# Kernel optimization log

Measured on AMD Instinct MI355X. Metric: run time of the kernel, lower is better.

Reference implementation:

```python
import jax, jax.numpy as jnp
import numpy as np

LEVELS = 2
BS = 8                 # block_size == plane_h == plane_w
NORMALS = (0, 1, 2)    # axis-aligned plane normals within each block
TAU = 0.05
INV_SQRT2 = 0.7071067811865476

# ---------- 1D orthonormal Haar along an axis ----------

def _dwt1(x, axis):
    x = jnp.moveaxis(x, axis, -1)
    a, b = x[..., 0::2], x[..., 1::2]
    lo = (a + b) * INV_SQRT2
    hi = (a - b) * INV_SQRT2
    return jnp.moveaxis(lo, -1, axis), jnp.moveaxis(hi, -1, axis)


def _idwt1(lo, hi, axis):
    lo = jnp.moveaxis(lo, axis, -1)
    hi = jnp.moveaxis(hi, axis, -1)
    even = (lo + hi) * INV_SQRT2
    odd = (lo - hi) * INV_SQRT2
    y = jnp.stack([even, odd], axis=-1).reshape(lo.shape[:-1] + (lo.shape[-1] * 2,))
    return jnp.moveaxis(y, -1, axis)

# ---------- one level of separable 3D Haar (8 subbands) ----------

def _dwt3_level(x):
    ld, hd = _dwt1(x, -3)
    out = {}
    for dn, db in (('l', ld), ('h', hd)):
        lh, hh = _dwt1(db, -2)
        for hn, hb in (('l', lh), ('h', hh)):
            lw, hw = _dwt1(hb, -1)
            out[dn + hn + 'l'] = lw
            out[dn + hn + 'h'] = hw
    return out


def _idwt3_level(bands):
    rec_h = {dn + hn: _idwt1(bands[dn + hn + 'l'], bands[dn + hn + 'h'], -1)
             for dn in 'lh' for hn in 'lh'}
    rec_d = {dn: _idwt1(rec_h[dn + 'l'], rec_h[dn + 'h'], -2) for dn in 'lh'}
    return _idwt1(rec_d['l'], rec_d['h'], -3)

# ---------- full multi-level 2D Haar on the last two dims (planes) ----------

def _haar2_fwd(p):
    s = p.shape[-1]
    out = p
    while s > 1:
        sub = out[..., :s, :s]
        a, b = sub[..., 0::2, :], sub[..., 1::2, :]
        sub = jnp.concatenate([(a + b) * INV_SQRT2, (a - b) * INV_SQRT2], axis=-2)
        a, b = sub[..., :, 0::2], sub[..., :, 1::2]
        sub = jnp.concatenate([(a + b) * INV_SQRT2, (a - b) * INV_SQRT2], axis=-1)
        out = out.at[..., :s, :s].set(sub)
        s //= 2
    return out


def _haar2_inv(c):
    s_full = c.shape[-1]
    out = c
    s = 2
    while s <= s_full:
        sub = out[..., :s, :s]
        lo, hi = sub[..., :, :s // 2], sub[..., :, s // 2:]
        even = (lo + hi) * INV_SQRT2
        odd = (lo - hi) * INV_SQRT2
        sub = jnp.stack([even, odd], axis=-1).reshape(sub.shape[:-1] + (s,))
        lo, hi = sub[..., :s // 2, :], sub[..., s // 2:, :]
        even = (lo + hi) * INV_SQRT2
        odd = (lo - hi) * INV_SQRT2
        sub = jnp.stack([even, odd], axis=-2).reshape(sub.shape[:-2] + (s, s))
        out = out.at[..., :s, :s].set(sub)
        s *= 2
    return out

# ---------- block extraction / assembly ----------

def _extract_blocks(band, bs):
    B, C, D, H, W = band.shape
    pd, ph, pw = (-D) % bs, (-H) % bs, (-W) % bs
    band = jnp.pad(band, ((0, 0), (0, 0), (0, pd), (0, ph), (0, pw)), mode='edge')
    nd, nh, nw = (D + pd) // bs, (H + ph) // bs, (W + pw) // bs
    blk = band.reshape(B, C, nd, bs, nh, bs, nw, bs).transpose(0, 1, 2, 4, 6, 3, 5, 7)
    return blk.reshape(-1, bs, bs, bs), (B, C, D, H, W), (nd, nh, nw)


def _assemble_blocks(blocks, orig, nblk, bs):
    B, C, D, H, W = orig
    nd, nh, nw = nblk
    x = blocks.reshape(B, C, nd, nh, nw, bs, bs, bs).transpose(0, 1, 2, 5, 3, 6, 4, 7)
    x = x.reshape(B, C, nd * bs, nh * bs, nw * bs)
    return x[:, :, :D, :H, :W]

# ---------- planewise bandlet analysis / synthesis ----------

def _analyze(blocks):
    # for each normal axis n: slice cube into planes perpendicular to n, 2D Haar each plane
    return jnp.stack([_haar2_fwd(jnp.moveaxis(blocks, 1 + n, 1)) for n in NORMALS], axis=1)


def _synthesize(packed):
    recs = [jnp.moveaxis(_haar2_inv(packed[:, i]), 1, 1 + n) for i, n in enumerate(NORMALS)]
    acc = recs[0]
    for r in recs[1:]:
        acc = acc + r
    return acc / len(NORMALS)


def _soft_threshold(c, tau):
    dc = c[..., 0, 0]  # keep per-plane DC coefficient
    t = jnp.sign(c) * jnp.maximum(jnp.abs(c) - tau, 0.0)
    return t.at[..., 0, 0].set(dc)

# ---------- full encode -> threshold -> reconstruct ----------

def _forward(x):
    B, C, D, H, W = x.shape
    mult = 2 ** LEVELS
    pd, ph, pw = (-D) % mult, (-H) % mult, (-W) % mult
    xp = jnp.pad(x, ((0, 0), (0, 0), (0, pd), (0, ph), (0, pw)), mode='reflect')
    approx = xp
    levels = []
    for _ in range(LEVELS):
        bands = _dwt3_level(approx)
        approx = bands.pop('lll')
        levels.append(bands)
    rec_levels = []
    for bands in levels:
        rec = {}
        for name, band in bands.items():
            blocks, orig, nblk = _extract_blocks(band, BS)
            packed = _soft_threshold(_analyze(blocks), TAU)
            rec[name] = _assemble_blocks(_synthesize(packed), orig, nblk, BS)
        rec_levels.append(rec)
    y = approx
    for bands in reversed(rec_levels):
        bands = dict(bands)
        bands['lll'] = y
        y = _idwt3_level(bands)
    return y[:, :, :D, :H, :W]


def setup_inputs() -> dict:
    key = jax.random.key(0)
    x = jax.random.normal(key, (2, 1, 160, 160, 160), dtype=jnp.float32)
    return {"x": x}


def reference(x):
    return _forward(x)
```

## Files before the change

kernel.cpp:

```cpp
#include <hip/hip_runtime.h>

#define IS2 0.7071067811865476f
#define C3F 0.35355339059327373f
#define TAU_F 0.05f

__device__ __forceinline__ void haar2_fwd(float (&m)[64]) {
    float t[64];
    #pragma unroll
    for (int half = 4; half >= 1; half >>= 1) {
        const int sz = half * 2;
        #pragma unroll
        for (int r = 0; r < half; ++r)
            #pragma unroll
            for (int c = 0; c < sz; ++c) {
                float a = m[(2*r)*8 + c], b = m[(2*r+1)*8 + c];
                t[r*8 + c]        = (a + b) * IS2;
                t[(r+half)*8 + c] = (a - b) * IS2;
            }
        #pragma unroll
        for (int r = 0; r < sz; ++r)
            #pragma unroll
            for (int c = 0; c < sz; ++c) m[r*8+c] = t[r*8+c];
        #pragma unroll
        for (int r = 0; r < sz; ++r)
            #pragma unroll
            for (int c = 0; c < half; ++c) {
                float a = m[r*8 + 2*c], b = m[r*8 + 2*c + 1];
                t[r*8 + c]        = (a + b) * IS2;
                t[r*8 + c + half] = (a - b) * IS2;
            }
        #pragma unroll
        for (int r = 0; r < sz; ++r)
            #pragma unroll
            for (int c = 0; c < sz; ++c) m[r*8+c] = t[r*8+c];
    }
}

__device__ __forceinline__ void haar2_inv(float (&m)[64]) {
    float t[64];
    #pragma unroll
    for (int sz = 2; sz <= 8; sz <<= 1) {
        const int half = sz >> 1;
        #pragma unroll
        for (int r = 0; r < sz; ++r)
            #pragma unroll
            for (int c = 0; c < half; ++c) {
                float lo = m[r*8 + c], hi = m[r*8 + c + half];
                t[r*8 + 2*c]     = (lo + hi) * IS2;
                t[r*8 + 2*c + 1] = (lo - hi) * IS2;
            }
        #pragma unroll
        for (int r = 0; r < sz; ++r)
            #pragma unroll
            for (int c = 0; c < sz; ++c) m[r*8+c] = t[r*8+c];
        #pragma unroll
        for (int r = 0; r < half; ++r)
            #pragma unroll
            for (int c = 0; c < sz; ++c) {
                float lo = m[r*8 + c], hi = m[(r+half)*8 + c];
                t[(2*r)*8 + c]   = (lo + hi) * IS2;
                t[(2*r+1)*8 + c] = (lo - hi) * IS2;
            }
        #pragma unroll
        for (int r = 0; r < sz; ++r)
            #pragma unroll
            for (int c = 0; c < sz; ++c) m[r*8+c] = t[r*8+c];
    }
}

__device__ __forceinline__ void bandlet_slice(float (&m)[64]) {
    haar2_fwd(m);
    float dc = m[0];
    #pragma unroll
    for (int e = 0; e < 64; ++e) {
        float v = m[e];
        float av = fabsf(v) - TAU_F;
        m[e] = av > 0.0f ? copysignf(av, v) : 0.0f;
    }
    m[0] = dc;
    haar2_inv(m);
}

__device__ __forceinline__ void bandlet_core(float* __restrict__ L, int s,
                                             bool valid, float (&a)[64]) {
    float g[64], w[64];
    if (valid) {
        #pragma unroll
        for (int r = 0; r < 8; ++r) {
            float4 v0 = *(const float4*)&L[s*64 + r*8];
            float4 v1 = *(const float4*)&L[s*64 + r*8 + 4];
            a[r*8+0]=v0.x; a[r*8+1]=v0.y; a[r*8+2]=v0.z; a[r*8+3]=v0.w;
            a[r*8+4]=v1.x; a[r*8+5]=v1.y; a[r*8+6]=v1.z; a[r*8+7]=v1.w;
        }
        bandlet_slice(a);
        #pragma unroll
        for (int r = 0; r < 8; ++r)
            #pragma unroll
            for (int c = 0; c < 8; ++c)
                g[r*8+c] = L[r*64 + c*8 + s];
        bandlet_slice(g);
        #pragma unroll
        for (int r = 0; r < 8; ++r) {
            float4 v0 = *(const float4*)&L[r*64 + s*8];
            float4 v1 = *(const float4*)&L[r*64 + s*8 + 4];
            w[r*8+0]=v0.x; w[r*8+1]=v0.y; w[r*8+2]=v0.z; w[r*8+3]=v0.w;
            w[r*8+4]=v1.x; w[r*8+5]=v1.y; w[r*8+6]=v1.z; w[r*8+7]=v1.w;
        }
    }
    __syncthreads();
    if (valid) {
        #pragma unroll
        for (int r = 0; r < 8; ++r)
            #pragma unroll
            for (int c = 0; c < 8; ++c)
                L[r*64 + c*8 + s] = g[r*8+c];
        bandlet_slice(w);
    }
    __syncthreads();
    if (valid) {
        #pragma unroll
        for (int r = 0; r < 8; ++r) {
            float4 v0 = *(const float4*)&L[s*64 + r*8];
            float4 v1 = *(const float4*)&L[s*64 + r*8 + 4];
            a[r*8+0]+=v0.x; a[r*8+1]+=v0.y; a[r*8+2]+=v0.z; a[r*8+3]+=v0.w;
            a[r*8+4]+=v1.x; a[r*8+5]+=v1.y; a[r*8+6]+=v1.z; a[r*8+7]+=v1.w;
        }
    }
    __syncthreads();
    if (valid) {
        #pragma unroll
        for (int r = 0; r < 8; ++r) {
            *(float4*)&L[r*64 + s*8]     = make_float4(w[r*8+0], w[r*8+1], w[r*8+2], w[r*8+3]);
            *(float4*)&L[r*64 + s*8 + 4] = make_float4(w[r*8+4], w[r*8+5], w[r*8+6], w[r*8+7]);
        }
    }
    __syncthreads();
    if (valid) {
        #pragma unroll
        for (int r = 0; r < 8; ++r) {
            float4 v0 = *(const float4*)&L[s*64 + r*8];
            float4 v1 = *(const float4*)&L[s*64 + r*8 + 4];
            a[r*8+0]+=v0.x; a[r*8+1]+=v0.y; a[r*8+2]+=v0.z; a[r*8+3]+=v0.w;
            a[r*8+4]+=v1.x; a[r*8+5]+=v1.y; a[r*8+6]+=v1.z; a[r*8+7]+=v1.w;
        }
    }
}

__global__ __launch_bounds__(64, 2) void fwd1_bp(const float* __restrict__ x,
                                                 float* __restrict__ bands) {
    constexpr int LST = 516;
    constexpr size_t B1S = (size_t)2 * 80 * 80 * 80;
    __shared__ __align__(16) float lin[7 * LST];

    const int t  = threadIdx.x;
    const int wg = blockIdx.x;
    const int b  = wg / 1000;
    const int tl = wg - b * 1000;
    const int td = tl / 100;
    const int rr = tl - td * 100;
    const int th = rr / 10;
    const int tw = rr - th * 10;
    const int j = t >> 3, w = t & 7;

    const float* ip = x + ((size_t)(b*160 + 16*td)) * 25600 + (size_t)(16*th) * 160 + 16*tw;
    float* lllp = bands + ((size_t)(b*80 + 8*td)) * 6400 + (size_t)(8*th) * 80 + 8*tw;

    #pragma unroll
    for (int q = 0; q < 8; ++q) {
        const float* p = ip + (size_t)(2*q) * 25600 + (2*j) * 160 + 2*w;
        float2 q00 = *(const float2*)(p);
        float2 q01 = *(const float2*)(p + 160);
        float2 q10 = *(const float2*)(p + 25600);
        float2 q11 = *(const float2*)(p + 25600 + 160);
        float wl00 = q00.x + q00.y, wh00 = q00.x - q00.y;
        float wl01 = q01.x + q01.y, wh01 = q01.x - q01.y;
        float wl10 = q10.x + q10.y, wh10 = q10.x - q10.y;
        float wl11 = q11.x + q11.y, wh11 = q11.x - q11.y;
        float hl0l = wl00 + wl01, hh0l = wl00 - wl01;
        float hl0h = wh00 + wh01, hh0h = wh00 - wh01;
        float hl1l = wl10 + wl11, hh1l = wl10 - wl11;
        float hl1h = wh10 + wh11, hh1h = wh10 - wh11;
        const int pos = q*64 + j*8 + w;
        lin[0*LST + pos] = (hl0h + hl1h) * C3F;
        lin[1*LST + pos] = (hh0l + hh1l) * C3F;
        lin[2*LST + pos] = (hh0h + hh1h) * C3F;
        lin[3*LST + pos] = (hl0l - hl1l) * C3F;
        lin[4*LST + pos] = (hl0h - hl1h) * C3F;
        lin[5*LST + pos] = (hh0l - hh1l) * C3F;
        lin[6*LST + pos] = (hh0h - hh1h) * C3F;
        lllp[q*6400 + j*80 + w] = (hl0l + hl1l) * C3F;
    }
    __syncthreads();

    const int nbp = t >> 3, s = t & 7;
    const bool valid = nbp < 7;
    float a[64];
    bandlet_core(&lin[(valid ? nbp : 0) * LST], s, valid, a);

    if (valid) {
        float* gp = bands + (size_t)(nbp + 1) * B1S
                  + ((size_t)(b*80 + 8*td + s)) * 6400 + (size_t)(8*th) * 80 + 8*tw;
        #pragma unroll
        for (int jj = 0; jj < 8; ++jj) {
            float* qo = gp + jj * 80;
            *(float4*)(qo)     = make_float4(a[jj*8+0]*(1.0f/3.0f), a[jj*8+1]*(1.0f/3.0f),
                                             a[jj*8+2]*(1.0f/3.0f), a[jj*8+3]*(1.0f/3.0f));
            *(float4*)(qo + 4) = make_float4(a[jj*8+4]*(1.0f/3.0f), a[jj*8+5]*(1.0f/3.0f),
                                             a[jj*8+6]*(1.0f/3.0f), a[jj*8+7]*(1.0f/3.0f));
        }
    }
}

__global__ __launch_bounds__(64, 2) void l2_pipeline(float* __restrict__ lll) {
    constexpr int LST = 516;
    __shared__ __align__(16) float lin[8 * LST];

    const int t  = threadIdx.x;
    const int wg = blockIdx.x;
    const int b  = wg / 125;
    const int tl = wg - b * 125;
    const int td = tl / 25;
    const int rr = tl - td * 25;
    const int th = rr / 5;
    const int tw = rr - th * 5;
    const int j = t >> 3, w = t & 7;

    float* base = lll + ((size_t)(b*80 + 16*td)) * 6400 + (size_t)(16*th) * 80 + 16*tw;

    #pragma unroll
    for (int q = 0; q < 8; ++q) {
        const float* p = base + (size_t)(2*q) * 6400 + (2*j) * 80 + 2*w;
        float2 q00 = *(const float2*)(p);
        float2 q01 = *(const float2*)(p + 80);
        float2 q10 = *(const float2*)(p + 6400);
        float2 q11 = *(const float2*)(p + 6400 + 80);
        float wl00 = q00.x + q00.y, wh00 = q00.x - q00.y;
        float wl01 = q01.x + q01.y, wh01 = q01.x - q01.y;
        float wl10 = q10.x + q10.y, wh10 = q10.x - q10.y;
        float wl11 = q11.x + q11.y, wh11 = q11.x - q11.y;
        float hl0l = wl00 + wl01, hh0l = wl00 - wl01;
        float hl0h = wh00 + wh01, hh0h = wh00 - wh01;
        float hl1l = wl10 + wl11, hh1l = wl10 - wl11;
        float hl1h = wh10 + wh11, hh1h = wh10 - wh11;
        const int pos = q*64 + j*8 + w;
        lin[0*LST + pos] = (hl0l + hl1l) * C3F;
        lin[1*LST + pos] = (hl0h + hl1h) * C3F;
        lin[2*LST + pos] = (hh0l + hh1l) * C3F;
        lin[3*LST + pos] = (hh0h + hh1h) * C3F;
        lin[4*LST + pos] = (hl0l - hl1l) * C3F;
        lin[5*LST + pos] = (hl0h - hl1h) * C3F;
        lin[6*LST + pos] = (hh0l - hh1l) * C3F;
        lin[7*LST + pos] = (hh0h - hh1h) * C3F;
    }
    __syncthreads();

    const int nbp = t >> 3, s = t & 7;
    const bool valid = nbp < 7;
    float a[64];
    bandlet_core(&lin[(valid ? nbp + 1 : 0) * LST], s, valid, a);

    __syncthreads();
    if (valid) {
        float* L = &lin[(nbp + 1) * LST];
        #pragma unroll
        for (int jj = 0; jj < 8; ++jj) {
            *(float4*)&L[s*64 + jj*8]     = make_float4(a[jj*8+0]*(1.0f/3.0f), a[jj*8+1]*(1.0f/3.0f),
                                                        a[jj*8+2]*(1.0f/3.0f), a[jj*8+3]*(1.0f/3.0f));
            *(float4*)&L[s*64 + jj*8 + 4] = make_float4(a[jj*8+4]*(1.0f/3.0f), a[jj*8+5]*(1.0f/3.0f),
                                                        a[jj*8+6]*(1.0f/3.0f), a[jj*8+7]*(1.0f/3.0f));
        }
    }
    __syncthreads();

    #pragma unroll
    for (int q = 0; q < 8; ++q) {
        const int pos = q*64 + j*8 + w;
        float b0 = lin[0*LST + pos], b1 = lin[1*LST + pos];
        float b2 = lin[2*LST + pos], b3 = lin[3*LST + pos];
        float b4 = lin[4*LST + pos], b5 = lin[5*LST + pos];
        float b6 = lin[6*LST + pos], b7 = lin[7*LST + pos];
        float c0 = b0 + b4, c1 = b1 + b5, c2 = b2 + b6, c3 = b3 + b7;
        float c4 = b0 - b4, c5 = b1 - b5, c6 = b2 - b6, c7 = b3 - b7;
        float e00 = c0 + c2, e01 = c1 + c3;
        float e02 = c0 - c2, e03 = c1 - c3;
        float e10 = c4 + c6, e11 = c5 + c7;
        float e12 = c4 - c6, e13 = c5 - c7;
        float* pp = base + (size_t)(2*q) * 6400 + (2*j) * 80 + 2*w;
        *(float2*)(pp)             = make_float2((e00+e01)*C3F, (e00-e01)*C3F);
        *(float2*)(pp + 80)        = make_float2((e02+e03)*C3F, (e02-e03)*C3F);
        *(float2*)(pp + 6400)      = make_float2((e10+e11)*C3F, (e10-e11)*C3F);
        *(float2*)(pp + 6400 + 80) = make_float2((e12+e13)*C3F, (e12-e13)*C3F);
    }
}

__global__ __launch_bounds__(256) void dwt3_inv80(const float* __restrict__ bands,
                                                  float* __restrict__ out) {
    const int tid = blockIdx.x * blockDim.x + threadIdx.x;
    constexpr int S = 80;
    const int w = tid % S;
    const int h = (tid / S) % S;
    const int d = (tid / (S*S)) % S;
    const int b = tid / (S*S*S);
    constexpr size_t bs_ = (size_t)2 * S * S * S;
    const size_t o = (size_t)tid;

    float b0 = bands[0*bs_+o], b1 = bands[1*bs_+o], b2 = bands[2*bs_+o], b3 = bands[3*bs_+o];
    float b4 = bands[4*bs_+o], b5 = bands[5*bs_+o], b6 = bands[6*bs_+o], b7 = bands[7*bs_+o];
    float c0 = b0 + b4, c1 = b1 + b5, c2 = b2 + b6, c3 = b3 + b7;
    float c4 = b0 - b4, c5 = b1 - b5, c6 = b2 - b6, c7 = b3 - b7;
    float e00 = c0 + c2, e01 = c1 + c3;
    float e02 = c0 - c2, e03 = c1 - c3;
    float e10 = c4 + c6, e11 = c5 + c7;
    float e12 = c4 - c6, e13 = c5 - c7;
    constexpr int IS = 2 * S;
    float* p = out + (((size_t)b * IS + 2*d) * IS + 2*h) * IS + 2*w;
    *(float2*)(p)                      = make_float2((e00+e01)*C3F, (e00-e01)*C3F);
    *(float2*)(p + IS)                 = make_float2((e02+e03)*C3F, (e02-e03)*C3F);
    *(float2*)(p + (size_t)IS*IS)      = make_float2((e10+e11)*C3F, (e10-e11)*C3F);
    *(float2*)(p + (size_t)IS*IS + IS) = make_float2((e12+e13)*C3F, (e12-e13)*C3F);
}

extern "C" void kernel_launch(void* const* d_in, const int* in_sizes, int n_in,
                              void* d_out, int out_size, void* d_ws, size_t ws_size,
                              hipStream_t stream) {
    const float* x = (const float*)d_in[0];
    float* out = (float*)d_out;
    float* bands = (float*)d_ws;

    fwd1_bp<<<2000, 64, 0, stream>>>(x, bands);
    l2_pipeline<<<250, 64, 0, stream>>>(bands);
    dwt3_inv80<<<4000, 256, 0, stream>>>(bands, out);
}
```

Before: 119.3 us.

## Split three bandlet orientations across three wavefronts and widen inverse DWT per thread

Each workgroup now runs 192 threads, so each of the three plane orientations of the bandlet transform gets its own wavefront instead of one thread processing all three serially. The second orientation's result is routed through an extra shared buffer and summed by wave 0. The Haar 2D transforms use smaller temporaries to cut register pressure. The final inverse DWT processes two outputs per thread with float2 loads and float4 stores. Shared memory per block roughly doubles, and 8 of every 64 lanes in each wave stay idle, which may limit occupancy.

New measurement: 120.3 us. No clear change (+0.8%).

```diff
diff --git a/kernel.cpp b/kernel.cpp
--- a/kernel.cpp
+++ b/kernel.cpp
@@ -3,68 +3,68 @@
 #define IS2 0.7071067811865476f
 #define C3F 0.35355339059327373f
 #define TAU_F 0.05f
+#define THIRD 0.3333333333333333f
 
 __device__ __forceinline__ void haar2_fwd(float (&m)[64]) {
-    float t[64];
     #pragma unroll
     for (int half = 4; half >= 1; half >>= 1) {
         const int sz = half * 2;
+        float th[32];
         #pragma unroll
         for (int r = 0; r < half; ++r)
             #pragma unroll
             for (int c = 0; c < sz; ++c) {
                 float a = m[(2*r)*8 + c], b = m[(2*r+1)*8 + c];
-                t[r*8 + c]        = (a + b) * IS2;
-                t[(r+half)*8 + c] = (a - b) * IS2;
-            }
-        #pragma unroll
-        for (int r = 0; r < sz; ++r)
-            #pragma unroll
-            for (int c = 0; c < sz; ++c) m[r*8+c] = t[r*8+c];
-        #pragma unroll
-        for (int r = 0; r < sz; ++r)
+                m[r*8 + c] = (a + b) * IS2;
+                th[r*8 + c] = (a - b) * IS2;
+            }
+        #pragma unroll
+        for (int r = 0; r < half; ++r)
+            #pragma unroll
+            for (int c = 0; c < sz; ++c) m[(r+half)*8 + c] = th[r*8 + c];
+        #pragma unroll
+        for (int r = 0; r < sz; ++r) {
+            float tw[4];
             #pragma unroll
             for (int c = 0; c < half; ++c) {
                 float a = m[r*8 + 2*c], b = m[r*8 + 2*c + 1];
-                t[r*8 + c]        = (a + b) * IS2;
-                t[r*8 + c + half] = (a - b) * IS2;
-            }
-        #pragma unroll
-        for (int r = 0; r < sz; ++r)
-            #pragma unroll
-            for (int c = 0; c < sz; ++c) m[r*8+c] = t[r*8+c];
+                m[r*8 + c] = (a + b) * IS2;
+                tw[c]      = (a - b) * IS2;
+            }
+            #pragma unroll
+            for (int c = 0; c < half; ++c) m[r*8 + c + half] = tw[c];
+        }
     }
 }
 
 __device__ __forceinline__ void haar2_inv(float (&m)[64]) {
-    float t[64];
     #pragma unroll
     for (int sz = 2; sz <= 8; sz <<= 1) {
         const int half = sz >> 1;
         #pragma unroll
-        for (int r = 0; r < sz; ++r)
+        for (int r = 0; r < sz; ++r) {
+            float te[8];
             #pragma unroll
             for (int c = 0; c < half; ++c) {
                 float lo = m[r*8 + c], hi = m[r*8 + c + half];
-                t[r*8 + 2*c]     = (lo + hi) * IS2;
-                t[r*8 + 2*c + 1] = (lo - hi) * IS2;
-            }
-        #pragma unroll
-        for (int r = 0; r < sz; ++r)
-            #pragma unroll
-            for (int c = 0; c < sz; ++c) m[r*8+c] = t[r*8+c];
-        #pragma unroll
-        for (int r = 0; r < half; ++r)
-            #pragma unroll
-            for (int c = 0; c < sz; ++c) {
+                te[2*c]   = (lo + hi) * IS2;
+                te[2*c+1] = (lo - hi) * IS2;
+            }
+            #pragma unroll
+            for (int k = 0; k < sz; ++k) m[r*8 + k] = te[k];
+        }
+        #pragma unroll
+        for (int c = 0; c < sz; ++c) {
+            float tc[8];
+            #pragma unroll
+            for (int r = 0; r < half; ++r) {
                 float lo = m[r*8 + c], hi = m[(r+half)*8 + c];
-                t[(2*r)*8 + c]   = (lo + hi) * IS2;
-                t[(2*r+1)*8 + c] = (lo - hi) * IS2;
-            }
-        #pragma unroll
-        for (int r = 0; r < sz; ++r)
-            #pragma unroll
-            for (int c = 0; c < sz; ++c) m[r*8+c] = t[r*8+c];
+                tc[2*r]   = (lo + hi) * IS2;
+                tc[2*r+1] = (lo - hi) * IS2;
+            }
+            #pragma unroll
+            for (int r = 0; r < sz; ++r) m[r*8 + c] = tc[r];
+        }
     }
 }
 
@@ -81,76 +81,74 @@
     haar2_inv(m);
 }
 
-__device__ __forceinline__ void bandlet_core(float* __restrict__ L, int s,
-                                             bool valid, float (&a)[64]) {
-    float g[64], w[64];
-    if (valid) {
+__device__ __forceinline__ void blockproc3(float* __restrict__ Lb,
+                                           float* __restrict__ Rb,
+                                           int wv, int s, bool act,
+                                           float (&m)[64]) {
+    if (act) {
+        if (wv == 0) {
+            #pragma unroll
+            for (int r = 0; r < 8; ++r) {
+                float4 v0 = *(const float4*)&Lb[s*64 + r*8];
+                float4 v1 = *(const float4*)&Lb[s*64 + r*8 + 4];
+                m[r*8+0]=v0.x; m[r*8+1]=v0.y; m[r*8+2]=v0.z; m[r*8+3]=v0.w;
+                m[r*8+4]=v1.x; m[r*8+5]=v1.y; m[r*8+6]=v1.z; m[r*8+7]=v1.w;
+            }
+        } else if (wv == 1) {
+            #pragma unroll
+            for (int r = 0; r < 8; ++r) {
+                float4 v0 = *(const float4*)&Lb[r*64 + s*8];
+                float4 v1 = *(const float4*)&Lb[r*64 + s*8 + 4];
+                m[r*8+0]=v0.x; m[r*8+1]=v0.y; m[r*8+2]=v0.z; m[r*8+3]=v0.w;
+                m[r*8+4]=v1.x; m[r*8+5]=v1.y; m[r*8+6]=v1.z; m[r*8+7]=v1.w;
+            }
+        } else {
+            #pragma unroll
+            for (int r = 0; r < 8; ++r)
+                #pragma unroll
+                for (int c = 0; c < 8; ++c)
+                    m[r*8+c] = Lb[r*64 + c*8 + s];
+        }
+    }
+    __syncthreads();
+    if (act) {
+        bandlet_slice(m);
+        if (wv == 1) {
+            #pragma unroll
+            for (int r = 0; r < 8; ++r) {
+                *(float4*)&Lb[r*64 + s*8]     = make_float4(m[r*8+0], m[r*8+1], m[r*8+2], m[r*8+3]);
+                *(float4*)&Lb[r*64 + s*8 + 4] = make_float4(m[r*8+4], m[r*8+5], m[r*8+6], m[r*8+7]);
+            }
+        } else if (wv == 2) {
+            #pragma unroll
+            for (int r = 0; r < 8; ++r)
+                #pragma unroll
+                for (int c = 0; c < 8; ++c)
+                    Rb[r*64 + c*8 + s] = m[r*8+c];
+        }
+    }
+    __syncthreads();
+    if (act && wv == 0) {
         #pragma unroll
         for (int r = 0; r < 8; ++r) {
-            float4 v0 = *(const float4*)&L[s*64 + r*8];
-            float4 v1 = *(const float4*)&L[s*64 + r*8 + 4];
-            a[r*8+0]=v0.x; a[r*8+1]=v0.y; a[r*8+2]=v0.z; a[r*8+3]=v0.w;
-            a[r*8+4]=v1.x; a[r*8+5]=v1.y; a[r*8+6]=v1.z; a[r*8+7]=v1.w;
-        }
-        bandlet_slice(a);
-        #pragma unroll
-        for (int r = 0; r < 8; ++r)
-            #pragma unroll
-            for (int c = 0; c < 8; ++c)
-                g[r*8+c] = L[r*64 + c*8 + s];
-        bandlet_slice(g);
-        #pragma unroll
-        for (int r = 0; r < 8; ++r) {
-            float4 v0 = *(const float4*)&L[r*64 + s*8];
-            float4 v1 = *(const float4*)&L[r*64 + s*8 + 4];
-            w[r*8+0]=v0.x; w[r*8+1]=v0.y; w[r*8+2]=v0.z; w[r*8+3]=v0.w;
-            w[r*8+4]=v1.x; w[r*8+5]=v1.y; w[r*8+6]=v1.z; w[r*8+7]=v1.w;
-        }
-    }
-    __syncthreads();
-    if (valid) {
-        #pragma unroll
-        for (int r = 0; r < 8; ++r)
-            #pragma unroll
-            for (int c = 0; c < 8; ++c)
-                L[r*64 + c*8 + s] = g[r*8+c];
-        bandlet_slice(w);
-    }
-    __syncthreads();
-    if (valid) {
-        #pragma unroll
-        for (int r = 0; r < 8; ++r) {
-            float4 v0 = *(const float4*)&L[s*64 + r*8];
-            float4 v1 = *(const float4*)&L[s*64 + r*8 + 4];
-            a[r*8+0]+=v0.x; a[r*8+1]+=v0.y; a[r*8+2]+=v0.z; a[r*8+3]+=v0.w;
-            a[r*8+4]+=v1.x; a[r*8+5]+=v1.y; a[r*8+6]+=v1.z; a[r*8+7]+=v1.w;
-        }
-    }
-    __syncthreads();
-    if (valid) {
-        #pragma unroll
-        for (int r = 0; r < 8; ++r) {
-            *(float4*)&L[r*64 + s*8]     = make_float4(w[r*8+0], w[r*8+1], w[r*8+2], w[r*8+3]);
-            *(float4*)&L[r*64 + s*8 + 4] = make_float4(w[r*8+4], w[r*8+5], w[r*8+6], w[r*8+7]);
-        }
-    }
-    __syncthreads();
-    if (valid) {
-        #pragma unroll
-        for (int r = 0; r < 8; ++r) {
-            float4 v0 = *(const float4*)&L[s*64 + r*8];
-            float4 v1 = *(const float4*)&L[s*64 + r*8 + 4];
-            a[r*8+0]+=v0.x; a[r*8+1]+=v0.y; a[r*8+2]+=v0.z; a[r*8+3]+=v0.w;
-            a[r*8+4]+=v1.x; a[r*8+5]+=v1.y; a[r*8+6]+=v1.z; a[r*8+7]+=v1.w;
-        }
-    }
-}
-
-__global__ __launch_bounds__(64, 2) void fwd1_bp(const float* __restrict__ x,
-                                                 float* __restrict__ bands) {
+            float4 a0 = *(const float4*)&Lb[s*64 + r*8];
+            float4 a1 = *(const float4*)&Lb[s*64 + r*8 + 4];
+            float4 b0 = *(const float4*)&Rb[s*64 + r*8];
+            float4 b1 = *(const float4*)&Rb[s*64 + r*8 + 4];
+            m[r*8+0] += a0.x + b0.x; m[r*8+1] += a0.y + b0.y;
+            m[r*8+2] += a0.z + b0.z; m[r*8+3] += a0.w + b0.w;
+            m[r*8+4] += a1.x + b1.x; m[r*8+5] += a1.y + b1.y;
+            m[r*8+6] += a1.z + b1.z; m[r*8+7] += a1.w + b1.w;
+        }
+    }
+}
+
+__global__ __launch_bounds__(192, 4) void fwd1_bp(const float* __restrict__ x,
+                                                  float* __restrict__ bands) {
     constexpr int LST = 516;
     constexpr size_t B1S = (size_t)2 * 80 * 80 * 80;
     __shared__ __align__(16) float lin[7 * LST];
+    __shared__ __align__(16) float lr2[7 * LST];
 
     const int t  = threadIdx.x;
     const int wg = blockIdx.x;
@@ -160,60 +158,69 @@
     const int rr = tl - td * 100;
     const int th = rr / 10;
     const int tw = rr - th * 10;
-    const int j = t >> 3, w = t & 7;
 
     const float* ip = x + ((size_t)(b*160 + 16*td)) * 25600 + (size_t)(16*th) * 160 + 16*tw;
     float* lllp = bands + ((size_t)(b*80 + 8*td)) * 6400 + (size_t)(8*th) * 80 + 8*tw;
 
     #pragma unroll
-    for (int q = 0; q < 8; ++q) {
-        const float* p = ip + (size_t)(2*q) * 25600 + (2*j) * 160 + 2*w;
-        float2 q00 = *(const float2*)(p);
-        float2 q01 = *(const float2*)(p + 160);
-        float2 q10 = *(const float2*)(p + 25600);
-        float2 q11 = *(const float2*)(p + 25600 + 160);
-        float wl00 = q00.x + q00.y, wh00 = q00.x - q00.y;
-        float wl01 = q01.x + q01.y, wh01 = q01.x - q01.y;
-        float wl10 = q10.x + q10.y, wh10 = q10.x - q10.y;
-        float wl11 = q11.x + q11.y, wh11 = q11.x - q11.y;
-        float hl0l = wl00 + wl01, hh0l = wl00 - wl01;
-        float hl0h = wh00 + wh01, hh0h = wh00 - wh01;
-        float hl1l = wl10 + wl11, hh1l = wl10 - wl11;
-        float hl1h = wh10 + wh11, hh1h = wh10 - wh11;
-        const int pos = q*64 + j*8 + w;
-        lin[0*LST + pos] = (hl0h + hl1h) * C3F;
-        lin[1*LST + pos] = (hh0l + hh1l) * C3F;
-        lin[2*LST + pos] = (hh0h + hh1h) * C3F;
-        lin[3*LST + pos] = (hl0l - hl1l) * C3F;
-        lin[4*LST + pos] = (hl0h - hl1h) * C3F;
-        lin[5*LST + pos] = (hh0l - hh1l) * C3F;
-        lin[6*LST + pos] = (hh0h - hh1h) * C3F;
-        lllp[q*6400 + j*80 + w] = (hl0l + hl1l) * C3F;
-    }
-    __syncthreads();
-
-    const int nbp = t >> 3, s = t & 7;
-    const bool valid = nbp < 7;
-    float a[64];
-    bandlet_core(&lin[(valid ? nbp : 0) * LST], s, valid, a);
-
-    if (valid) {
-        float* gp = bands + (size_t)(nbp + 1) * B1S
+    for (int k = 0; k < 3; ++k) {
+        const int p = t + k * 192;
+        if (p < 512) {
+            const int q = p >> 6, j = (p >> 3) & 7, w = p & 7;
+            const float* pp = ip + (size_t)(2*q) * 25600 + (2*j) * 160 + 2*w;
+            float2 q00 = *(const float2*)(pp);
+            float2 q01 = *(const float2*)(pp + 160);
+            float2 q10 = *(const float2*)(pp + 25600);
+            float2 q11 = *(const float2*)(pp + 25600 + 160);
+            float wl00 = q00.x + q00.y, wh00 = q00.x - q00.y;
+            float wl01 = q01.x + q01.y, wh01 = q01.x - q01.y;
+            float wl10 = q10.x + q10.y, wh10 = q10.x - q10.y;
+            float wl11 = q11.x + q11.y, wh11 = q11.x - q11.y;
+            float hl0l = wl00 + wl01, hh0l = wl00 - wl01;
+            float hl0h = wh00 + wh01, hh0h = wh00 - wh01;
+            float hl1l = wl10 + wl11, hh1l = wl10 - wl11;
+            float hl1h = wh10 + wh11, hh1h = wh10 - wh11;
+            const int pos = q*64 + j*8 + w;
+            lin[0*LST + pos] = (hl0h + hl1h) * C3F;
+            lin[1*LST + pos] = (hh0l + hh1l) * C3F;
+            lin[2*LST + pos] = (hh0h + hh1h) * C3F;
+            lin[3*LST + pos] = (hl0l - hl1l) * C3F;
+            lin[4*LST + pos] = (hl0h - hl1h) * C3F;
+            lin[5*LST + pos] = (hh0l - hh1l) * C3F;
+            lin[6*LST + pos] = (hh0h - hh1h) * C3F;
+            lllp[q*6400 + j*80 + w] = (hl0l + hl1l) * C3F;
+        }
+    }
+    __syncthreads();
+
+    const int wv   = t >> 6;
+    const int lane = t & 63;
+    const int f    = lane >> 3;
+    const int s    = lane & 7;
+    const bool act = f < 7;
+    const int fc   = act ? f : 0;
+
+    float m[64];
+    blockproc3(&lin[fc * LST], &lr2[fc * LST], wv, s, act, m);
+
+    if (act && wv == 0) {
+        float* gp = bands + (size_t)(f + 1) * B1S
                   + ((size_t)(b*80 + 8*td + s)) * 6400 + (size_t)(8*th) * 80 + 8*tw;
         #pragma unroll
         for (int jj = 0; jj < 8; ++jj) {
             float* qo = gp + jj * 80;
-            *(float4*)(qo)     = make_float4(a[jj*8+0]*(1.0f/3.0f), a[jj*8+1]*(1.0f/3.0f),
-                                             a[jj*8+2]*(1.0f/3.0f), a[jj*8+3]*(1.0f/3.0f));
-            *(float4*)(qo + 4) = make_float4(a[jj*8+4]*(1.0f/3.0f), a[jj*8+5]*(1.0f/3.0f),
-                                             a[jj*8+6]*(1.0f/3.0f), a[jj*8+7]*(1.0f/3.0f));
-        }
-    }
-}
-
-__global__ __launch_bounds__(64, 2) void l2_pipeline(float* __restrict__ lll) {
+            *(float4*)(qo)     = make_float4(m[jj*8+0]*THIRD, m[jj*8+1]*THIRD,
+                                             m[jj*8+2]*THIRD, m[jj*8+3]*THIRD);
+            *(float4*)(qo + 4) = make_float4(m[jj*8+4]*THIRD, m[jj*8+5]*THIRD,
+                                             m[jj*8+6]*THIRD, m[jj*8+7]*THIRD);
+        }
+    }
+}
+
+__global__ __launch_bounds__(192, 4) void l2_pipeline(float* __restrict__ lll) {
     constexpr int LST = 516;
     __shared__ __align__(16) float lin[8 * LST];
+    __shared__ __align__(16) float lr2[7 * LST];
 
     const int t  = threadIdx.x;
     const int wg = blockIdx.x;
@@ -223,73 +230,83 @@
     const int rr = tl - td * 25;
     const int th = rr / 5;
     const int tw = rr - th * 5;
-    const int j = t >> 3, w = t & 7;
 
     float* base = lll + ((size_t)(b*80 + 16*td)) * 6400 + (size_t)(16*th) * 80 + 16*tw;
 
     #pragma unroll
-    for (int q = 0; q < 8; ++q) {
-        const float* p = base + (size_t)(2*q) * 6400 + (2*j) * 80 + 2*w;
-        float2 q00 = *(const float2*)(p);
-        float2 q01 = *(const float2*)(p + 80);
-        float2 q10 = *(const float2*)(p + 6400);
-        float2 q11 = *(const float2*)(p + 6400 + 80);
-        float wl00 = q00.x + q00.y, wh00 = q00.x - q00.y;
-        float wl01 = q01.x + q01.y, wh01 = q01.x - q01.y;
-        float wl10 = q10.x + q10.y, wh10 = q10.x - q10.y;
-        float wl11 = q11.x + q11.y, wh11 = q11.x - q11.y;
-        float hl0l = wl00 + wl01, hh0l = wl00 - wl01;
-        float hl0h = wh00 + wh01, hh0h = wh00 - wh01;
-        float hl1l = wl10 + wl11, hh1l = wl10 - wl11;
-        float hl1h = wh10 + wh11, hh1h = wh10 - wh11;
-        const int pos = q*64 + j*8 + w;
-        lin[0*LST + pos] = (hl0l + hl1l) * C3F;
-        lin[1*LST + pos] = (hl0h + hl1h) * C3F;
-        lin[2*LST + pos] = (hh0l + hh1l) * C3F;
-        lin[3*LST + pos] = (hh0h + hh1h) * C3F;
-        lin[4*LST + pos] = (hl0l - hl1l) * C3F;
-        lin[5*LST + pos] = (hl0h - hl1h) * C3F;
-        lin[6*LST + pos] = (hh0l - hh1l) * C3F;
-        lin[7*LST + pos] = (hh0h - hh1h) * C3F;
-    }
-    __syncthreads();
-
-    const int nbp = t >> 3, s = t & 7;
-    const bool valid = nbp < 7;
-    float a[64];
-    bandlet_core(&lin[(valid ? nbp + 1 : 0) * LST], s, valid, a);
-
-    __syncthreads();
-    if (valid) {
-        float* L = &lin[(nbp + 1) * LST];
-        #pragma unroll
-        for (int jj = 0; jj < 8; ++jj) {
-            *(float4*)&L[s*64 + jj*8]     = make_float4(a[jj*8+0]*(1.0f/3.0f), a[jj*8+1]*(1.0f/3.0f),
-                                                        a[jj*8+2]*(1.0f/3.0f), a[jj*8+3]*(1.0f/3.0f));
-            *(float4*)&L[s*64 + jj*8 + 4] = make_float4(a[jj*8+4]*(1.0f/3.0f), a[jj*8+5]*(1.0f/3.0f),
-                                                        a[jj*8+6]*(1.0f/3.0f), a[jj*8+7]*(1.0f/3.0f));
-        }
-    }
-    __syncthreads();
-
-    #pragma unroll
-    for (int q = 0; q < 8; ++q) {
-        const int pos = q*64 + j*8 + w;
-        float b0 = lin[0*LST + pos], b1 = lin[1*LST + pos];
-        float b2 = lin[2*LST + pos], b3 = lin[3*LST + pos];
-        float b4 = lin[4*LST + pos], b5 = lin[5*LST + pos];
-        float b6 = lin[6*LST + pos], b7 = lin[7*LST + pos];
-        float c0 = b0 + b4, c1 = b1 + b5, c2 = b2 + b6, c3 = b3 + b7;
-        float c4 = b0 - b4, c5 = b1 - b5, c6 = b2 - b6, c7 = b3 - b7;
-        float e00 = c0 + c2, e01 = c1 + c3;
-        float e02 = c0 - c2, e03 = c1 - c3;
-        float e10 = c4 + c6, e11 = c5 + c7;
-        float e12 = c4 - c6, e13 = c5 - c7;
-        float* pp = base + (size_t)(2*q) * 6400 + (2*j) * 80 + 2*w;
-        *(float2*)(pp)             = make_float2((e00+e01)*C3F, (e00-e01)*C3F);
-        *(float2*)(pp + 80)        = make_float2((e02+e03)*C3F, (e02-e03)*C3F);
-        *(float2*)(pp + 6400)      = make_float2((e10+e11)*C3F, (e10-e11)*C3F);
-        *(float2*)(pp + 6400 + 80) = make_float2((e12+e13)*C3F, (e12-e13)*C3F);
+    for (int k = 0; k < 3; ++k) {
+        const int p = t + k * 192;
+        if (p < 512) {
+            const int q = p >> 6, j = (p >> 3) & 7, w = p & 7;
+            const float* pp = base + (size_t)(2*q) * 6400 + (2*j) * 80 + 2*w;
+            float2 q00 = *(const float2*)(pp);
+            float2 q01 = *(const float2*)(pp + 80);
+            float2 q10 = *(const float2*)(pp + 6400);
+            float2 q11 = *(const float2*)(pp + 6400 + 80);
+            float wl00 = q00.x + q00.y, wh00 = q00.x - q00.y;
+            float wl01 = q01.x + q01.y, wh01 = q01.x - q01.y;
+            float wl10 = q10.x + q10.y, wh10 = q10.x - q10.y;
+            float wl11 = q11.x + q11.y, wh11 = q11.x - q11.y;
+            float hl0l = wl00 + wl01, hh0l = wl00 - wl01;
+            float hl0h = wh00 + wh01, hh0h = wh00 - wh01;
+            float hl1l = wl10 + wl11, hh1l = wl10 - wl11;
+            float hl1h = wh10 + wh11, hh1h = wh10 - wh11;
+            const int pos = q*64 + j*8 + w;
+            lin[0*LST + pos] = (hl0l + hl1l) * C3F;
+            lin[1*LST + pos] = (hl0h + hl1h) * C3F;
+            lin[2*LST + pos] = (hh0l + hh1l) * C3F;
+            lin[3*LST + pos] = (hh0h + hh1h) * C3F;
+            lin[4*LST + pos] = (hl0l - hl1l) * C3F;
+            lin[5*LST + pos] = (hl0h - hl1h) * C3F;
+            lin[6*LST + pos] = (hh0l - hh1l) * C3F;
+            lin[7*LST + pos] = (hh0h - hh1h) * C3F;
+        }
+    }
+    __syncthreads();
+
+    const int wv   = t >> 6;
+    const int lane = t & 63;
+    const int f    = lane >> 3;
+    const int s    = lane & 7;
+    const bool act = f < 7;
+
+    float m[64];
+    blockproc3(&lin[(act ? f + 1 : 1) * LST], &lr2[(act ? f : 0) * LST], wv, s, act, m);
+
+    if (act && wv == 0) {
+        float* Lb = &lin[(f + 1) * LST];
+        #pragma unroll
+        for (int r = 0; r < 8; ++r) {
+            *(float4*)&Lb[s*64 + r*8]     = make_float4(m[r*8+0]*THIRD, m[r*8+1]*THIRD,
+                                                        m[r*8+2]*THIRD, m[r*8+3]*THIRD);
+            *(float4*)&Lb[s*64 + r*8 + 4] = make_float4(m[r*8+4]*THIRD, m[r*8+5]*THIRD,
+                                                        m[r*8+6]*THIRD, m[r*8+7]*THIRD);
+        }
+    }
+    __syncthreads();
+
+    #pragma unroll
+    for (int k = 0; k < 3; ++k) {
+        const int p = t + k * 192;
+        if (p < 512) {
+            const int q = p >> 6, j = (p >> 3) & 7, w = p & 7;
+            const int pos = q*64 + j*8 + w;
+            float b0 = lin[0*LST + pos], b1 = lin[1*LST + pos];
+            float b2 = lin[2*LST + pos], b3 = lin[3*LST + pos];
+            float b4 = lin[4*LST + pos], b5 = lin[5*LST + pos];
+            float b6 = lin[6*LST + pos], b7 = lin[7*LST + pos];
+            float c0 = b0 + b4, c1 = b1 + b5, c2 = b2 + b6, c3 = b3 + b7;
+            float c4 = b0 - b4, c5 = b1 - b5, c6 = b2 - b6, c7 = b3 - b7;
+            float e00 = c0 + c2, e01 = c1 + c3;
+            float e02 = c0 - c2, e03 = c1 - c3;
+            float e10 = c4 + c6, e11 = c5 + c7;
+            float e12 = c4 - c6, e13 = c5 - c7;
+            float* pp = base + (size_t)(2*q) * 6400 + (2*j) * 80 + 2*w;
+            *(float2*)(pp)             = make_float2((e00+e01)*C3F, (e00-e01)*C3F);
+            *(float2*)(pp + 80)        = make_float2((e02+e03)*C3F, (e02-e03)*C3F);
+            *(float2*)(pp + 6400)      = make_float2((e10+e11)*C3F, (e10-e11)*C3F);
+            *(float2*)(pp + 6400 + 80) = make_float2((e12+e13)*C3F, (e12-e13)*C3F);
+        }
     }
 }
 
@@ -297,27 +314,41 @@
                                                   float* __restrict__ out) {
     const int tid = blockIdx.x * blockDim.x + threadIdx.x;
     constexpr int S = 80;
-    const int w = tid % S;
-    const int h = (tid / S) % S;
-    const int d = (tid / (S*S)) % S;
-    const int b = tid / (S*S*S);
     constexpr size_t bs_ = (size_t)2 * S * S * S;
-    const size_t o = (size_t)tid;
-
-    float b0 = bands[0*bs_+o], b1 = bands[1*bs_+o], b2 = bands[2*bs_+o], b3 = bands[3*bs_+o];
-    float b4 = bands[4*bs_+o], b5 = bands[5*bs_+o], b6 = bands[6*bs_+o], b7 = bands[7*bs_+o];
-    float c0 = b0 + b4, c1 = b1 + b5, c2 = b2 + b6, c3 = b3 + b7;
-    float c4 = b0 - b4, c5 = b1 - b5, c6 = b2 - b6, c7 = b3 - b7;
-    float e00 = c0 + c2, e01 = c1 + c3;
-    float e02 = c0 - c2, e03 = c1 - c3;
-    float e10 = c4 + c6, e11 = c5 + c7;
-    float e12 = c4 - c6, e13 = c5 - c7;
-    constexpr int IS = 2 * S;
-    float* p = out + (((size_t)b * IS + 2*d) * IS + 2*h) * IS + 2*w;
-    *(float2*)(p)                      = make_float2((e00+e01)*C3F, (e00-e01)*C3F);
-    *(float2*)(p + IS)                 = make_float2((e02+e03)*C3F, (e02-e03)*C3F);
-    *(float2*)(p + (size_t)IS*IS)      = make_float2((e10+e11)*C3F, (e10-e11)*C3F);
-    *(float2*)(p + (size_t)IS*IS + IS) = make_float2((e12+e13)*C3F, (e12-e13)*C3F);
+    const size_t o = (size_t)tid * 2;
+    const int w = (int)(o % S);
+    const int h = (int)((o / S) % S);
+    const int d = (int)((o / (S*S)) % S);
+    const int b = (int)(o / ((size_t)S*S*S));
+
+    float2 B0 = *(const float2*)&bands[0*bs_ + o];
+    float2 B1 = *(const float2*)&bands[1*bs_ + o];
+    float2 B2 = *(const float2*)&bands[2*bs_ + o];
+    float2 B3 = *(const float2*)&bands[3*bs_ + o];
+    float2 B4 = *(const float2*)&bands[4*bs_ + o];
+    float2 B5 = *(const float2*)&bands[5*bs_ + o];
+    float2 B6 = *(const float2*)&bands[6*bs_ + o];
+    float2 B7 = *(const float2*)&bands[7*bs_ + o];
+
+    float c0x = B0.x + B4.x, c1x = B1.x + B5.x, c2x = B2.x + B6.x, c3x = B3.x + B7.x;
+    float c4x = B0.x - B4.x, c5x = B1.x - B5.x, c6x = B2.x - B6.x, c7x = B3.x - B7.x;
+    float e00x = c0x + c2x, e01x = c1x + c3x, e02x = c0x - c2x, e03x = c1x - c3x;
+    float e10x = c4x + c6x, e11x = c5x + c7x, e12x = c4x - c6x, e13x = c5x - c7x;
+
+    float c0y = B0.y + B4.y, c1y = B1.y + B5.y, c2y = B2.y + B6.y, c3y = B3.y + B7.y;
+    float c4y = B0.y - B4.y, c5y = B1.y - B5.y, c6y = B2.y - B6.y, c7y = B3.y - B7.y;
+    float e00y = c0y + c2y, e01y = c1y + c3y, e02y = c0y - c2y, e03y = c1y - c3y;
+    float e10y = c4y + c6y, e11y = c5y + c7y, e12y = c4y - c6y, e13y = c5y - c7y;
+
+    float* p = out + (((size_t)b * 160 + 2*d) * 160 + 2*h) * 160 + 2*w;
+    *(float4*)(p)               = make_float4((e00x+e01x)*C3F, (e00x-e01x)*C3F,
+                                              (e00y+e01y)*C3F, (e00y-e01y)*C3F);
+    *(float4*)(p + 160)         = make_float4((e02x+e03x)*C3F, (e02x-e03x)*C3F,
+                                              (e02y+e03y)*C3F, (e02y-e03y)*C3F);
+    *(float4*)(p + 25600)       = make_float4((e10x+e11x)*C3F, (e10x-e11x)*C3F,
+                                              (e10y+e11y)*C3F, (e10y-e11y)*C3F);
+    *(float4*)(p + 25600 + 160) = make_float4((e12x+e13x)*C3F, (e12x-e13x)*C3F,
+                                              (e12y+e13y)*C3F, (e12y-e13y)*C3F);
 }
 
 extern "C" void kernel_launch(void* const* d_in, const int* in_sizes, int n_in,
@@ -327,7 +358,7 @@
     float* out = (float*)d_out;
     float* bands = (float*)d_ws;
 
-    fwd1_bp<<<2000, 64, 0, stream>>>(x, bands);
-    l2_pipeline<<<250, 64, 0, stream>>>(bands);
-    dwt3_inv80<<<4000, 256, 0, stream>>>(bands, out);
-}
+    fwd1_bp<<<2000, 192, 0, stream>>>(x, bands);
+    l2_pipeline<<<250, 192, 0, stream>>>(bands);
+    dwt3_inv80<<<2000, 256, 0, stream>>>(bands, out);
+}
```
